# Performance work log

Measured on AMD Instinct MI355X. Metric: run time of the kernel, lower is better.

Reference implementation:

```python
import jax, jax.numpy as jnp
import numpy as np

DIM = 1024
N_HEADS = 16
HEAD_DIM = DIM // N_HEADS
B, N, M = 2, 2048, 2048


def setup_inputs() -> dict:
    key = jax.random.key(0)
    ks = jax.random.split(key, 10)
    s = 1.0 / np.sqrt(DIM)
    return {
        "x1": jax.random.normal(ks[0], (B, N, DIM), dtype=jnp.float32),
        "x2": jax.random.normal(ks[1], (B, M, DIM), dtype=jnp.float32),
        "Wq": jax.random.normal(ks[2], (DIM, DIM), dtype=jnp.float32) * s,
        "bq": jnp.zeros((DIM,), dtype=jnp.float32),
        "Wk": jax.random.normal(ks[3], (DIM, DIM), dtype=jnp.float32) * s,
        "bk": jnp.zeros((DIM,), dtype=jnp.float32),
        "Wv": jax.random.normal(ks[4], (DIM, DIM), dtype=jnp.float32) * s,
        "bv": jnp.zeros((DIM,), dtype=jnp.float32),
        "Wo": jax.random.normal(ks[5], (DIM, DIM), dtype=jnp.float32) * s,
        "bo": jnp.zeros((DIM,), dtype=jnp.float32),
    }


def reference(x1, x2, Wq, bq, Wk, bk, Wv, bv, Wo, bo):
    b, n, _ = x1.shape
    m = x2.shape[1]
    # projections (Linear: x @ W^T + b)
    q = x1 @ Wq.T + bq  # [b, n, dim]
    k = x2 @ Wk.T + bk  # [b, m, dim]
    v = x2 @ Wv.T + bv  # [b, m, dim]
    # split heads -> [b, h, seq, head_dim]
    q = q.reshape(b, n, N_HEADS, HEAD_DIM).transpose(0, 2, 1, 3)
    k = k.reshape(b, m, N_HEADS, HEAD_DIM).transpose(0, 2, 1, 3)
    v = v.reshape(b, m, N_HEADS, HEAD_DIM).transpose(0, 2, 1, 3)
    scale = 1.0 / jnp.sqrt(jnp.asarray(HEAD_DIM, dtype=q.dtype))
    scores = jnp.einsum('bhnd,bhmd->bhnm', q, k) * scale  # [b, h, n, m]
    attn = jax.nn.softmax(scores, axis=-1)
    o = jnp.einsum('bhnm,bhmd->bhnd', attn, v)  # [b, h, n, head_dim]
    o = o.transpose(0, 2, 1, 3).reshape(b, n, DIM)  # merge heads
    return o @ Wo.T + bo
```

## Files before the change

### kernel.cpp

```cpp
#include <hip/hip_runtime.h>
#include <stdint.h>

typedef unsigned short u16;
typedef __attribute__((ext_vector_type(4))) float f32x4;
typedef __attribute__((ext_vector_type(8))) __bf16 bf16x8;
typedef __attribute__((ext_vector_type(8))) unsigned short u16x8;
typedef __attribute__((ext_vector_type(4))) unsigned short u16x4;

#define DIM_    1024
#define NHEADS_ 16
#define HD_     64
#define BB_     2
#define NN_     2048
#define MM_     2048

#define QSCALE 0.180336884f

__device__ inline u16 f32_to_bf16u(float f) {
  union { float f; uint32_t u; } x; x.f = f;
  uint32_t r = x.u + 0x7FFFu + ((x.u >> 16) & 1u);
  return (u16)(r >> 16);
}

__device__ inline void gload_lds16(const u16* g, u16* l) {
  u16* gnc = const_cast<u16*>(g);
  __builtin_amdgcn_global_load_lds(
      (__attribute__((address_space(1))) void*)gnc,
      (__attribute__((address_space(3))) void*)l, 16, 0, 0);
}

__global__ void cast_all(const float* s0, u16* d0, const float* s1, u16* d1,
                         const float* s2, u16* d2, const float* s3, u16* d3,
                         const float* s4, u16* d4, const float* s5, u16* d5) {
  const float* s; u16* d; int n4;
  switch (blockIdx.y) {
    case 0: s = s0; d = d0; n4 = (BB_ * NN_ * DIM_) / 4; break;
    case 1: s = s1; d = d1; n4 = (BB_ * MM_ * DIM_) / 4; break;
    case 2: s = s2; d = d2; n4 = (DIM_ * DIM_) / 4; break;
    case 3: s = s3; d = d3; n4 = (DIM_ * DIM_) / 4; break;
    case 4: s = s4; d = d4; n4 = (DIM_ * DIM_) / 4; break;
    default: s = s5; d = d5; n4 = (DIM_ * DIM_) / 4; break;
  }
  int stride = gridDim.x * blockDim.x;
  for (int i = blockIdx.x * blockDim.x + threadIdx.x; i < n4; i += stride) {
    float4 f = reinterpret_cast<const float4*>(s)[i];
    u16x4 u;
    u.x = f32_to_bf16u(f.x);
    u.y = f32_to_bf16u(f.y);
    u.z = f32_to_bf16u(f.z);
    u.w = f32_to_bf16u(f.w);
    reinterpret_cast<u16x4*>(d)[i] = u;
  }
}

#define BM 128
#define BN 128
#define BK 64

template <bool BF16OUT>
__device__ __forceinline__
void gemm_body(const u16* __restrict__ A, const u16* __restrict__ Bm,
               const float* __restrict__ bias, void* __restrict__ Cout,
               int M, int N, int K, float scale,
               u16* As , u16* Bs ) {
  const int tid  = threadIdx.x;
  const int lane = tid & 63;
  const int wid  = tid >> 6;
  const int wr = wid >> 2, wc = wid & 3;
  const int fr = lane & 15, fq = lane >> 4;
  const int bm = blockIdx.x, bn = blockIdx.y;
  const int lrow = lane >> 3;
  const int scol = (((lane & 7) ^ lrow) * 8);

  f32x4 acc[4][2];
  #pragma unroll
  for (int m = 0; m < 4; ++m)
    #pragma unroll
    for (int n = 0; n < 2; ++n)
      acc[m][n] = f32x4{0.f, 0.f, 0.f, 0.f};

  const int NT = K / BK;

  auto stage = [&](int buf, int t) {
    int k0 = t * BK;
    #pragma unroll
    for (int c = 0; c < 2; ++c) {
      int ch  = wid * 2 + c;
      int row = ch * 8 + lrow;
      gload_lds16(A  + (size_t)(bm * BM + row) * K + k0 + scol, &As[buf * BM * BK + ch * 512]);
      gload_lds16(Bm + (size_t)(bn * BN + row) * K + k0 + scol, &Bs[buf * BN * BK + ch * 512]);
    }
  };

  stage(0, 0);
  __syncthreads();
  int cur = 0;
  for (int t = 0; t < NT; ++t) {
    if (t + 1 < NT) stage(cur ^ 1, t + 1);
    #pragma unroll
    for (int ks = 0; ks < 2; ++ks) {
      bf16x8 af[4], bfr[2];
      #pragma unroll
      for (int m = 0; m < 4; ++m)
        af[m] = *reinterpret_cast<const bf16x8*>(
            &As[cur * BM * BK + (wr * 64 + m * 16 + fr) * BK + (((ks * 4 + fq) ^ (fr & 7)) * 8)]);
      #pragma unroll
      for (int n = 0; n < 2; ++n)
        bfr[n] = *reinterpret_cast<const bf16x8*>(
            &Bs[cur * BN * BK + (wc * 32 + n * 16 + fr) * BK + (((ks * 4 + fq) ^ (fr & 7)) * 8)]);
      __builtin_amdgcn_s_setprio(1);
      #pragma unroll
      for (int m = 0; m < 4; ++m)
        #pragma unroll
        for (int n = 0; n < 2; ++n)
          acc[m][n] = __builtin_amdgcn_mfma_f32_16x16x32_bf16(af[m], bfr[n], acc[m][n], 0, 0, 0);
      __builtin_amdgcn_s_setprio(0);
    }
    __syncthreads();
    cur ^= 1;
  }

  #pragma unroll
  for (int n = 0; n < 2; ++n) {
    int col = bn * BN + wc * 32 + n * 16 + fr;
    float bv = bias[col];
    #pragma unroll
    for (int m = 0; m < 4; ++m) {
      #pragma unroll
      for (int i = 0; i < 4; ++i) {
        int row = bm * BM + wr * 64 + m * 16 + fq * 4 + i;
        float v = (acc[m][n][i] + bv) * scale;
        if (BF16OUT)
          ((u16*)Cout)[(size_t)row * N + col] = f32_to_bf16u(v);
        else
          ((float*)Cout)[(size_t)row * N + col] = v;
      }
    }
  }
}

__global__ __launch_bounds__(512)
void gemm_qkv(const u16* __restrict__ x1b, const u16* __restrict__ x2b,
              const u16* __restrict__ Wqb, const float* __restrict__ bq, u16* qb,
              const u16* __restrict__ Wkb, const float* __restrict__ bk, u16* kb,
              const u16* __restrict__ Wvb, const float* __restrict__ bv, u16* vb) {
  __shared__ __align__(16) u16 As[2 * BM * BK];
  __shared__ __align__(16) u16 Bs[2 * BN * BK];
  const u16* A; const u16* W; const float* bias; u16* C; float scale;
  switch (blockIdx.z) {
    case 0:  A = x1b; W = Wqb; bias = bq; C = qb; scale = QSCALE; break;
    case 1:  A = x2b; W = Wkb; bias = bk; C = kb; scale = 1.0f;   break;
    default: A = x2b; W = Wvb; bias = bv; C = vb; scale = 1.0f;   break;
  }
  gemm_body<true>(A, W, bias, C, BB_ * NN_, DIM_, DIM_, scale, As, Bs);
}

__global__ __launch_bounds__(512)
void gemm_o(const u16* __restrict__ A, const u16* __restrict__ W,
            const float* __restrict__ bias, float* __restrict__ C) {
  __shared__ __align__(16) u16 As[2 * BM * BK];
  __shared__ __align__(16) u16 Bs[2 * BN * BK];
  gemm_body<false>(A, W, bias, C, BB_ * NN_, DIM_, DIM_, 1.0f, As, Bs);
}

#define QB 128
#define KVB 64

__global__ __launch_bounds__(512)
void attn_fwd(const u16* __restrict__ qg, const u16* __restrict__ kg,
              const u16* __restrict__ vg, u16* __restrict__ og) {
  __shared__ __align__(16) u16 Ks[2][KVB * HD_];
  __shared__ __align__(16) u16 VTs[2][HD_ * KVB];
  __shared__ __align__(16) u16 Ps[8][16 * KVB];
  const int tid = threadIdx.x, lane = tid & 63, wid = tid >> 6;
  const int fr = lane & 15, fq = lane >> 4;
  const int b = blockIdx.z, h = blockIdx.y;
  const int q0 = blockIdx.x * QB + wid * 16;
  const size_t base_q  = (size_t)b * NN_ * DIM_ + (size_t)h * HD_;
  const size_t base_kv = (size_t)b * MM_ * DIM_ + (size_t)h * HD_;
  const int lrow = lane >> 3;
  const int scol = (((lane & 7) ^ lrow) * 8);
  const int ksw = (fr & 7);
  const int psw = (fr & 7) ^ (fr >> 3);

  bf16x8 qf[2];
  #pragma unroll
  for (int ks = 0; ks < 2; ++ks)
    qf[ks] = *reinterpret_cast<const bf16x8*>(qg + base_q + (size_t)(q0 + fr) * DIM_ + ks * 32 + fq * 8);

  bf16x8 onesf;
  #pragma unroll
  for (int j = 0; j < 8; ++j) onesf[j] = (__bf16)1.0f;

  f32x4 oacc[4];
  #pragma unroll
  for (int db = 0; db < 4; ++db) oacc[db] = f32x4{0.f, 0.f, 0.f, 0.f};
  f32x4 lacc = f32x4{0.f, 0.f, 0.f, 0.f};

  const int NT = MM_ / KVB;

  auto stageK = [&](int buf, int t) {
    int kv0 = t * KVB;
    int row = wid * 8 + lrow;
    gload_lds16(kg + base_kv + (size_t)(kv0 + row) * DIM_ + scol, &Ks[buf][wid * 512]);
  };
  auto loadV = [&](int t, u16x8& vpre) {
    int kv0 = t * KVB;
    vpre = *reinterpret_cast<const u16x8*>(vg + base_kv + (size_t)(kv0 + lane) * DIM_ + wid * 8);
  };
  auto writeVT = [&](int buf, const u16x8& vpre) {
    #pragma unroll
    for (int j = 0; j < 8; ++j)
      VTs[buf][(wid * 8 + j) * KVB + (((lane >> 3) ^ j) * 8) + (lane & 7)] = vpre[j];
  };

  {
    u16x8 v0;
    loadV(0, v0);
    stageK(0, 0);
    writeVT(0, v0);
    __syncthreads();
  }

  int cur = 0;
  u16* Pw = Ps[wid];
  for (int t = 0; t < NT; ++t) {
    u16x8 vpre;
    if (t + 1 < NT) {
      loadV(t + 1, vpre);
      stageK(cur ^ 1, t + 1);
    }

    f32x4 s[4];
    #pragma unroll
    for (int nb = 0; nb < 4; ++nb) s[nb] = f32x4{0.f, 0.f, 0.f, 0.f};
    __builtin_amdgcn_s_setprio(1);
    #pragma unroll
    for (int nb = 0; nb < 4; ++nb)
      #pragma unroll
      for (int ks = 0; ks < 2; ++ks) {
        bf16x8 kf = *reinterpret_cast<const bf16x8*>(
            &Ks[cur][(nb * 16 + fr) * HD_ + (((ks * 4 + fq) ^ ksw) * 8)]);
        s[nb] = __builtin_amdgcn_mfma_f32_16x16x32_bf16(qf[ks], kf, s[nb], 0, 0, 0);
      }
    __builtin_amdgcn_s_setprio(0);

    #pragma unroll
    for (int i = 0; i < 4; ++i) {
      const int q = fq * 4 + i;
      const int wkey = (q & 7) ^ (q >> 3);
      #pragma unroll
      for (int nb = 0; nb < 4; ++nb) {
        float p = __builtin_amdgcn_exp2f(s[nb][i]);
        Pw[q * KVB + (((nb * 2 + (fr >> 3)) ^ wkey) * 8) + (fr & 7)] = f32_to_bf16u(p);
      }
    }

    __builtin_amdgcn_s_setprio(1);
    #pragma unroll
    for (int ks = 0; ks < 2; ++ks) {
      bf16x8 pf = *reinterpret_cast<const bf16x8*>(
          &Pw[fr * KVB + (((ks * 4 + fq) ^ psw) * 8)]);
      lacc = __builtin_amdgcn_mfma_f32_16x16x32_bf16(pf, onesf, lacc, 0, 0, 0);
      #pragma unroll
      for (int db = 0; db < 4; ++db) {
        bf16x8 vf = *reinterpret_cast<const bf16x8*>(
            &VTs[cur][(db * 16 + fr) * KVB + (((ks * 4 + fq) ^ ksw) * 8)]);
        oacc[db] = __builtin_amdgcn_mfma_f32_16x16x32_bf16(pf, vf, oacc[db], 0, 0, 0);
      }
    }
    __builtin_amdgcn_s_setprio(0);

    if (t + 1 < NT) writeVT(cur ^ 1, vpre);
    __syncthreads();
    cur ^= 1;
  }

  #pragma unroll
  for (int i = 0; i < 4; ++i) {
    float inv = 1.f / lacc[i];
    size_t rowoff = base_q + (size_t)(q0 + fq * 4 + i) * DIM_;
    #pragma unroll
    for (int db = 0; db < 4; ++db)
      og[rowoff + db * 16 + fr] = f32_to_bf16u(oacc[db][i] * inv);
  }
}

extern "C" void kernel_launch(void* const* d_in, const int* in_sizes, int n_in,
                              void* d_out, int out_size, void* d_ws, size_t ws_size,
                              hipStream_t stream) {
  (void)in_sizes; (void)n_in; (void)out_size; (void)ws_size;
  const float* x1 = (const float*)d_in[0];
  const float* x2 = (const float*)d_in[1];
  const float* Wq = (const float*)d_in[2];
  const float* bq = (const float*)d_in[3];
  const float* Wk = (const float*)d_in[4];
  const float* bk = (const float*)d_in[5];
  const float* Wv = (const float*)d_in[6];
  const float* bv = (const float*)d_in[7];
  const float* Wo = (const float*)d_in[8];
  const float* bo = (const float*)d_in[9];
  float* out = (float*)d_out;

  char* ws = (char*)d_ws;
  u16* x1b = (u16*)(ws);
  u16* x2b = (u16*)(ws + (8u  << 20));
  u16* Wqb = (u16*)(ws + (16u << 20));
  u16* Wkb = (u16*)(ws + (18u << 20));
  u16* Wvb = (u16*)(ws + (20u << 20));
  u16* Wob = (u16*)(ws + (22u << 20));
  u16* qb  = (u16*)(ws + (24u << 20));
  u16* kb  = (u16*)(ws + (32u << 20));
  u16* vb  = (u16*)(ws + (40u << 20));
  u16* ob  = (u16*)(ws + (48u << 20));

  cast_all<<<dim3(512, 6), 256, 0, stream>>>(x1, x1b, x2, x2b, Wq, Wqb,
                                             Wk, Wkb, Wv, Wvb, Wo, Wob);

  const int Mrows = BB_ * NN_;
  dim3 gqkv(Mrows / BM, DIM_ / BN, 3);
  gemm_qkv<<<gqkv, 512, 0, stream>>>(x1b, x2b, Wqb, bq, qb, Wkb, bk, kb, Wvb, bv, vb);

  dim3 ga(NN_ / QB, NHEADS_, BB_);
  attn_fwd<<<ga, 512, 0, stream>>>(qb, kb, vb, ob);

  dim3 gg(Mrows / BM, DIM_ / BN);
  gemm_o<<<gg, 512, 0, stream>>>(ob, Wob, bo, out);
}
```

Before: 132.9 us.

## Process two KV tiles per barrier, remap blocks per XCD, pack P stores

```diff
diff --git a/kernel.cpp b/kernel.cpp
--- a/kernel.cpp
+++ b/kernel.cpp
@@ -4,6 +4,7 @@
 typedef unsigned short u16;
 typedef __attribute__((ext_vector_type(4))) float f32x4;
 typedef __attribute__((ext_vector_type(8))) __bf16 bf16x8;
+typedef __attribute__((ext_vector_type(4))) __bf16 bf16x4;
 typedef __attribute__((ext_vector_type(8))) unsigned short u16x8;
 typedef __attribute__((ext_vector_type(4))) unsigned short u16x4;
 
@@ -169,13 +170,19 @@
 __global__ __launch_bounds__(512)
 void attn_fwd(const u16* __restrict__ qg, const u16* __restrict__ kg,
               const u16* __restrict__ vg, u16* __restrict__ og) {
-  __shared__ __align__(16) u16 Ks[2][KVB * HD_];
-  __shared__ __align__(16) u16 VTs[2][HD_ * KVB];
+  __shared__ __align__(16) u16 Ks[4][KVB * HD_];
+  __shared__ __align__(16) u16 VTs[4][HD_ * KVB];
   __shared__ __align__(16) u16 Ps[8][16 * KVB];
   const int tid = threadIdx.x, lane = tid & 63, wid = tid >> 6;
   const int fr = lane & 15, fq = lane >> 4;
-  const int b = blockIdx.z, h = blockIdx.y;
-  const int q0 = blockIdx.x * QB + wid * 16;
+
+  int lin = blockIdx.x + gridDim.x * (blockIdx.y + gridDim.y * blockIdx.z);
+  int xcd = lin & 7, slot = lin >> 3;
+  int r = slot & 15, gg = slot >> 4;
+  int g = xcd + 8 * gg;
+  int h = g & 15, b = g >> 4;
+
+  const int q0 = r * QB + wid * 16;
   const size_t base_q  = (size_t)b * NN_ * DIM_ + (size_t)h * HD_;
   const size_t base_kv = (size_t)b * MM_ * DIM_ + (size_t)h * HD_;
   const int lrow = lane >> 3;
@@ -214,23 +221,9 @@
       VTs[buf][(wid * 8 + j) * KVB + (((lane >> 3) ^ j) * 8) + (lane & 7)] = vpre[j];
   };
 
-  {
-    u16x8 v0;
-    loadV(0, v0);
-    stageK(0, 0);
-    writeVT(0, v0);
-    __syncthreads();
-  }
-
-  int cur = 0;
   u16* Pw = Ps[wid];
-  for (int t = 0; t < NT; ++t) {
-    u16x8 vpre;
-    if (t + 1 < NT) {
-      loadV(t + 1, vpre);
-      stageK(cur ^ 1, t + 1);
-    }
-
+
+  auto compute = [&](int buf) {
     f32x4 s[4];
     #pragma unroll
     for (int nb = 0; nb < 4; ++nb) s[nb] = f32x4{0.f, 0.f, 0.f, 0.f};
@@ -240,20 +233,19 @@
       #pragma unroll
       for (int ks = 0; ks < 2; ++ks) {
         bf16x8 kf = *reinterpret_cast<const bf16x8*>(
-            &Ks[cur][(nb * 16 + fr) * HD_ + (((ks * 4 + fq) ^ ksw) * 8)]);
-        s[nb] = __builtin_amdgcn_mfma_f32_16x16x32_bf16(qf[ks], kf, s[nb], 0, 0, 0);
+            &Ks[buf][(nb * 16 + fr) * HD_ + (((ks * 4 + fq) ^ ksw) * 8)]);
+        s[nb] = __builtin_amdgcn_mfma_f32_16x16x32_bf16(kf, qf[ks], s[nb], 0, 0, 0);
       }
     __builtin_amdgcn_s_setprio(0);
 
     #pragma unroll
-    for (int i = 0; i < 4; ++i) {
-      const int q = fq * 4 + i;
-      const int wkey = (q & 7) ^ (q >> 3);
-      #pragma unroll
-      for (int nb = 0; nb < 4; ++nb) {
-        float p = __builtin_amdgcn_exp2f(s[nb][i]);
-        Pw[q * KVB + (((nb * 2 + (fr >> 3)) ^ wkey) * 8) + (fr & 7)] = f32_to_bf16u(p);
-      }
+    for (int nb = 0; nb < 4; ++nb) {
+      bf16x4 pk;
+      #pragma unroll
+      for (int i = 0; i < 4; ++i)
+        pk[i] = (__bf16)__builtin_amdgcn_exp2f(s[nb][i]);
+      *reinterpret_cast<bf16x4*>(
+          &Pw[fr * KVB + (((2 * nb + (fq >> 1)) ^ psw) * 8) + (fq & 1) * 4]) = pk;
     }
 
     __builtin_amdgcn_s_setprio(1);
@@ -265,15 +257,41 @@
       #pragma unroll
       for (int db = 0; db < 4; ++db) {
         bf16x8 vf = *reinterpret_cast<const bf16x8*>(
-            &VTs[cur][(db * 16 + fr) * KVB + (((ks * 4 + fq) ^ ksw) * 8)]);
+            &VTs[buf][(db * 16 + fr) * KVB + (((ks * 4 + fq) ^ ksw) * 8)]);
         oacc[db] = __builtin_amdgcn_mfma_f32_16x16x32_bf16(pf, vf, oacc[db], 0, 0, 0);
       }
     }
     __builtin_amdgcn_s_setprio(0);
-
-    if (t + 1 < NT) writeVT(cur ^ 1, vpre);
+  };
+
+  {
+    u16x8 v0, v1;
+    loadV(0, v0);
+    loadV(1, v1);
+    stageK(0, 0);
+    stageK(1, 1);
+    writeVT(0, v0);
+    writeVT(1, v1);
     __syncthreads();
-    cur ^= 1;
+  }
+
+  for (int it = 0; it < NT / 2; ++it) {
+    int t0 = 2 * it;
+    u16x8 vpre0, vpre1;
+    bool pre = (t0 + 2 < NT);
+    if (pre) {
+      loadV(t0 + 2, vpre0);
+      loadV(t0 + 3, vpre1);
+      stageK((t0 + 2) & 3, t0 + 2);
+      stageK((t0 + 3) & 3, t0 + 3);
+    }
+    compute(t0 & 3);
+    compute((t0 + 1) & 3);
+    if (pre) {
+      writeVT((t0 + 2) & 3, vpre0);
+      writeVT((t0 + 3) & 3, vpre1);
+    }
+    __syncthreads();
   }
 
   #pragma unroll
```

Measured after the change: 121.9 us. 8.2% less time.
